# Performance work log

Measured on AMD Instinct MI355X. Metric: run time of the kernel, lower is better.

The kernel has to match this reference:

```python
import jax, jax.numpy as jnp
import numpy as np

B, N, D = 1, 2048, 320
H, DH = 8, 40            # MultiheadAttention(320, num_heads=8)
STEPS, LR = 100, 0.01    # refinement_steps, refinement_lr
B1, B2, EPS = 0.9, 0.999, 1e-8  # torch Adam defaults


def setup_inputs() -> dict:
    key = jax.random.key(0)
    ks = iter(jax.random.split(key, 30))
    W = lambda shape: jax.random.normal(next(ks), shape, dtype=jnp.float32) * 0.05
    return {
        "features": jax.random.normal(next(ks), (B, N, D), dtype=jnp.float32),
        # backbone_network: Linear(320,320) ReLU Dropout Linear(320,320)
        "bb_w1": W((320, 320)), "bb_b1": W((320,)),
        "bb_w2": W((320, 320)), "bb_b2": W((320,)),
        # side_chain_network: Linear(320,160) ReLU Dropout Linear(160,320)
        "sc_w1": W((320, 160)), "sc_b1": W((160,)),
        "sc_w2": W((160, 320)), "sc_b2": W((320,)),
        # MultiheadAttention packed in/out projections
        "attn_wqkv": W((320, 960)), "attn_bqkv": W((960,)),
        "attn_wo": W((320, 320)), "attn_bo": W((320,)),
        # contact mlp: Linear(320,160) ReLU Linear(160,1)
        "cm_w1": W((320, 160)), "cm_b1": W((160,)),
        "cm_w2": W((160, 1)), "cm_b2": W((1,)),
        # refiner backbone_processor: Linear(320,160) ReLU Dropout Linear(160,3)
        "rb_w1": W((320, 160)), "rb_b1": W((160,)),
        "rb_w2": W((160, 3)), "rb_b2": W((3,)),
        # refiner side_chain_processor: Linear(320,160) ReLU Dropout Linear(160,4)
        "rs_w1": W((320, 160)), "rs_b1": W((160,)),
        "rs_w2": W((160, 4)), "rs_b2": W((4,)),
    }


def _mlp2(x, w1, b1, w2, b2):
    # Linear -> ReLU -> (Dropout eval = identity) -> Linear
    return jax.nn.relu(x @ w1 + b1) @ w2 + b2


def reference(features, bb_w1, bb_b1, bb_w2, bb_b2, sc_w1, sc_b1, sc_w2, sc_b2,
              attn_wqkv, attn_bqkv, attn_wo, attn_bo, cm_w1, cm_b1, cm_w2, cm_b2,
              rb_w1, rb_b1, rb_w2, rb_b2, rs_w1, rs_b1, rs_w2, rs_b2):
    backbone_features = _mlp2(features, bb_w1, bb_b1, bb_w2, bb_b2)       # (B,N,320)
    side_chain_features = _mlp2(backbone_features, sc_w1, sc_b1, sc_w2, sc_b2)

    # --- ContactMapPredictor (self-attention, batch-first) ---
    qkv = features @ attn_wqkv + attn_bqkv                                 # (B,N,960)
    q, k, v = jnp.split(qkv, 3, axis=-1)
    hsplit = lambda t: t.reshape(B, N, H, DH)
    scores = jnp.einsum('bqhd,bkhd->bhqk', hsplit(q), hsplit(k)) / jnp.sqrt(jnp.float32(DH))
    attn = jax.nn.softmax(scores, axis=-1)
    ctx = jnp.einsum('bhqk,bkhd->bqhd', attn, hsplit(v)).reshape(B, N, D)
    attn_out = ctx @ attn_wo + attn_bo                                     # (B,N,320)
    # torch loop writes a single scalar mlp(attn_out[:, i]) across each row i
    prob = jax.nn.relu(attn_out @ cm_w1 + cm_b1) @ cm_w2 + cm_b2           # (B,N,1)
    contact_map = jnp.broadcast_to(prob, (B, N, N))                        # (B,N,N)

    # --- StructureRefiner ---
    structure0 = _mlp2(backbone_features, rb_w1, rb_b1, rb_w2, rb_b2)      # (B,N,3)
    _side_chain_angles = _mlp2(side_chain_features, rs_w1, rs_b1, rs_w2, rs_b2)  # computed (unused downstream, as in source)

    def loss_fn(x):
        diffs = x[:, :, None, :] - x[:, None, :, :]                        # (B,N,N,3)
        dist = jnp.sqrt(jnp.sum(diffs * diffs, axis=-1) + 1e-12)
        contact_loss = jnp.mean(contact_map * jax.nn.relu(dist - 8.0)
                                + (1.0 - contact_map) * jax.nn.relu(12.0 - dist))
        bond = jnp.sqrt(jnp.sum((x[:, 1:] - x[:, :-1]) ** 2, axis=-1) + 1e-12)
        return contact_loss + 0.1 * jnp.mean(jax.nn.relu(bond - 4.0))

    @jax.checkpoint
    def step(carry, t):
        x, m, v = carry
        g = jax.grad(loss_fn)(x)
        m = B1 * m + (1.0 - B1) * g
        v = B2 * v + (1.0 - B2) * g * g
        mhat = m / (1.0 - B1 ** t)
        vhat = v / (1.0 - B2 ** t)
        x = x - LR * mhat / (jnp.sqrt(vhat) + EPS)
        return (x, m, v), None

    x0 = jax.lax.stop_gradient(structure0)  # torch: detach().clone() before optimization
    ts = jnp.arange(1, STEPS + 1, dtype=jnp.float32)
    (x, _, _), _ = jax.lax.scan(step, (x0, jnp.zeros_like(x0), jnp.zeros_like(x0)), ts)
    return x  # refined_structure (B,N,3)
```

## Files before the change

### kernel.cpp

```cpp
#include <hip/hip_runtime.h>
#include <math.h>

#define N_TOK 2048
#define NH 8
#define DH 40

__global__ __launch_bounds__(256) void gemm_k(const float* __restrict__ A,
    const float* __restrict__ B, const float* __restrict__ bias,
    float* __restrict__ C, int M, int N, int K, int relu)
{
    __shared__ __align__(16) float As[16][68];
    __shared__ __align__(16) float Bs[16][68];
    const int bn = blockIdx.x * 64, bm = blockIdx.y * 64;
    const int tid = threadIdx.x;
    const int tx = tid & 15, ty = tid >> 4;
    const int la_m = tid >> 2, la_k = (tid & 3) * 4;
    const int lb_k = tid >> 4, lb_n = (tid & 15) * 4;
    const int bcol = bn + lb_n;
    const int nk = K >> 4;
    float4 aq = *(const float4*)&A[(size_t)(bm + la_m) * K + la_k];
    float4 bq = make_float4(0.f, 0.f, 0.f, 0.f);
    if (bcol < N) bq = *(const float4*)&B[(size_t)lb_k * N + bcol];
    float acc[4][4] = {};
    for (int kt = 0; kt < nk; ++kt) {
        __syncthreads();
        As[la_k + 0][la_m] = aq.x; As[la_k + 1][la_m] = aq.y;
        As[la_k + 2][la_m] = aq.z; As[la_k + 3][la_m] = aq.w;
        *(float4*)&Bs[lb_k][lb_n] = bq;
        __syncthreads();
        if (kt + 1 < nk) {
            const int k0 = (kt + 1) << 4;
            aq = *(const float4*)&A[(size_t)(bm + la_m) * K + k0 + la_k];
            if (bcol < N) bq = *(const float4*)&B[(size_t)(k0 + lb_k) * N + bcol];
        }
        #pragma unroll
        for (int kk = 0; kk < 16; ++kk) {
            const float4 av = *(const float4*)&As[kk][4 * ty];
            const float4 bv = *(const float4*)&Bs[kk][4 * tx];
            acc[0][0] += av.x * bv.x; acc[0][1] += av.x * bv.y; acc[0][2] += av.x * bv.z; acc[0][3] += av.x * bv.w;
            acc[1][0] += av.y * bv.x; acc[1][1] += av.y * bv.y; acc[1][2] += av.y * bv.z; acc[1][3] += av.y * bv.w;
            acc[2][0] += av.z * bv.x; acc[2][1] += av.z * bv.y; acc[2][2] += av.z * bv.z; acc[2][3] += av.z * bv.w;
            acc[3][0] += av.w * bv.x; acc[3][1] += av.w * bv.y; acc[3][2] += av.w * bv.z; acc[3][3] += av.w * bv.w;
        }
    }
    const int c0 = bn + 4 * tx;
    if (c0 < N) {
        const float4 bz = *(const float4*)&bias[c0];
        #pragma unroll
        for (int i = 0; i < 4; ++i) {
            float4 o;
            o.x = acc[i][0] + bz.x; o.y = acc[i][1] + bz.y;
            o.z = acc[i][2] + bz.z; o.w = acc[i][3] + bz.w;
            if (relu) {
                o.x = fmaxf(o.x, 0.f); o.y = fmaxf(o.y, 0.f);
                o.z = fmaxf(o.z, 0.f); o.w = fmaxf(o.w, 0.f);
            }
            *(float4*)&C[(size_t)(bm + 4 * ty + i) * N + c0] = o;
        }
    }
}

__global__ __launch_bounds__(256) void mlp160_k(const float* __restrict__ X,
    const float* __restrict__ W1, const float* __restrict__ b1,
    const float* __restrict__ W2, const float* __restrict__ b2,
    float* __restrict__ out, int P)
{
    __shared__ __align__(16) float Xs[8][324];
    __shared__ float Hs[8][160];
    const int tid = threadIdx.x;
    const int r0 = blockIdx.x * 8;
    for (int idx = tid; idx < 8 * 80; idx += 256) {
        const int r = idx / 80, c4 = idx % 80;
        *(float4*)&Xs[r][4 * c4] = *(const float4*)&X[(size_t)(r0 + r) * 320 + 4 * c4];
    }
    __syncthreads();
    if (tid < 160) {
        const int c = tid;
        float a0 = 0.f, a1 = 0.f, a2 = 0.f, a3 = 0.f,
              a4 = 0.f, a5 = 0.f, a6 = 0.f, a7 = 0.f;
        #pragma unroll 4
        for (int k = 0; k < 320; ++k) {
            const float w = W1[(size_t)k * 160 + c];
            a0 = fmaf(Xs[0][k], w, a0); a1 = fmaf(Xs[1][k], w, a1);
            a2 = fmaf(Xs[2][k], w, a2); a3 = fmaf(Xs[3][k], w, a3);
            a4 = fmaf(Xs[4][k], w, a4); a5 = fmaf(Xs[5][k], w, a5);
            a6 = fmaf(Xs[6][k], w, a6); a7 = fmaf(Xs[7][k], w, a7);
        }
        const float bb = b1[c];
        Hs[0][c] = fmaxf(a0 + bb, 0.f); Hs[1][c] = fmaxf(a1 + bb, 0.f);
        Hs[2][c] = fmaxf(a2 + bb, 0.f); Hs[3][c] = fmaxf(a3 + bb, 0.f);
        Hs[4][c] = fmaxf(a4 + bb, 0.f); Hs[5][c] = fmaxf(a5 + bb, 0.f);
        Hs[6][c] = fmaxf(a6 + bb, 0.f); Hs[7][c] = fmaxf(a7 + bb, 0.f);
    }
    __syncthreads();
    const int r = tid >> 5, l = tid & 31;
    for (int p = 0; p < P; ++p) {
        float a = 0.f;
        for (int c = l; c < 160; c += 32)
            a = fmaf(Hs[r][c], W2[(size_t)c * P + p], a);
        #pragma unroll
        for (int off = 16; off; off >>= 1) a += __shfl_xor(a, off, 32);
        if (l == 0) out[(size_t)(r0 + r) * P + p] = a + b2[p];
    }
}

#define QT 16
#define KCH 2
#define KROWS (N_TOK / KCH)
__global__ __launch_bounds__(256) void attn_part_k(const float* __restrict__ qkv,
    float* __restrict__ ctxp, float* __restrict__ msp)
{
    __shared__ float Qs[DH][17];
    __shared__ __align__(16) float Ks[DH][64];
    __shared__ __align__(16) float Vs[DH][64];
    const int h = blockIdx.y;
    const int q0 = blockIdx.x * QT;
    const int ch = blockIdx.z;
    const int tid = threadIdx.x;
    const int kg = tid & 15, q = tid >> 4;

    for (int idx = tid; idx < QT * 10; idx += 256) {
        const int r = idx / 10, qd = idx % 10;
        const float4 qq = *(const float4*)&qkv[(size_t)(q0 + r) * 960 + h * DH + 4 * qd];
        Qs[4 * qd + 0][r] = qq.x; Qs[4 * qd + 1][r] = qq.y;
        Qs[4 * qd + 2][r] = qq.z; Qs[4 * qd + 3][r] = qq.w;
    }

    float M = -1e30f, S = 0.f;
    float ctx[DH];
    #pragma unroll
    for (int d = 0; d < DH; ++d) ctx[d] = 0.f;
    const float scale = 0.15811388300841897f;

    for (int t0 = ch * KROWS; t0 < (ch + 1) * KROWS; t0 += 64) {
        __syncthreads();
        for (int idx = tid; idx < 640; idx += 256) {
            const int r = idx / 10, qd = idx % 10;
            const float* base = &qkv[(size_t)(t0 + r) * 960 + h * DH];
            const float4 kq = *(const float4*)(base + 320 + 4 * qd);
            const float4 vq = *(const float4*)(base + 640 + 4 * qd);
            const int c = r ^ ((qd & 7) << 2);
            #pragma unroll
            for (int j = 0; j < 4; ++j) {
                const int d = 4 * qd + j;
                Ks[d][c] = ((const float*)&kq)[j];
                Vs[d][c] = ((const float*)&vq)[j];
            }
        }
        __syncthreads();

        float s0_ = 0.f, s1_ = 0.f, s2_ = 0.f, s3_ = 0.f;
        #pragma unroll
        for (int d = 0; d < DH; ++d) {
            const float qv = Qs[d][q];
            const float4 kv = *(const float4*)&Ks[d][(4 * kg) ^ (((d >> 2) & 7) << 2)];
            s0_ += qv * kv.x; s1_ += qv * kv.y; s2_ += qv * kv.z; s3_ += qv * kv.w;
        }
        s0_ *= scale; s1_ *= scale; s2_ *= scale; s3_ *= scale;

        float tm = fmaxf(fmaxf(s0_, s1_), fmaxf(s2_, s3_));
        #pragma unroll
        for (int off = 1; off < 16; off <<= 1) tm = fmaxf(tm, __shfl_xor(tm, off, 16));
        const float Mn = fmaxf(M, tm);
        const float p0 = __expf(s0_ - Mn), p1 = __expf(s1_ - Mn);
        const float p2 = __expf(s2_ - Mn), p3 = __expf(s3_ - Mn);
        float ps = p0 + p1 + p2 + p3;
        #pragma unroll
        for (int off = 1; off < 16; off <<= 1) ps += __shfl_xor(ps, off, 16);
        if (Mn > M) {
            const float sc = __expf(M - Mn);
            S = S * sc + ps; M = Mn;
            #pragma unroll
            for (int d = 0; d < DH; ++d) ctx[d] *= sc;
        } else S += ps;

        #pragma unroll
        for (int d = 0; d < DH; ++d) {
            const float4 vv = *(const float4*)&Vs[d][(4 * kg) ^ (((d >> 2) & 7) << 2)];
            ctx[d] += p0 * vv.x + p1 * vv.y + p2 * vv.z + p3 * vv.w;
        }
    }

    #pragma unroll
    for (int off = 1; off < 16; off <<= 1) {
        #pragma unroll
        for (int d = 0; d < DH; ++d) ctx[d] += __shfl_xor(ctx[d], off, 16);
    }
    const int qr = q0 + q;
    float4 o = make_float4(0.f, 0.f, 0.f, 0.f);
    #pragma unroll
    for (int qq = 0; qq < 10; ++qq) {
        if (kg == qq) {
            o.x = ctx[4 * qq + 0]; o.y = ctx[4 * qq + 1];
            o.z = ctx[4 * qq + 2]; o.w = ctx[4 * qq + 3];
        }
    }
    if (kg < 10)
        *(float4*)&ctxp[(size_t)((ch * N_TOK + qr) * NH + h) * DH + 4 * kg] = o;
    if (kg == 0)
        *(float2*)&msp[2 * ((size_t)(ch * N_TOK + qr) * NH + h)] = make_float2(M, S);
}

__global__ __launch_bounds__(320) void attn_comb_k(const float* __restrict__ ctxp,
    const float* __restrict__ msp, float* __restrict__ ctxo)
{
    const int q = blockIdx.x;
    const int t = threadIdx.x;
    const int h = t / DH, d = t % DH;
    const float2 ms0 = *(const float2*)&msp[2 * ((size_t)q * NH + h)];
    const float2 ms1 = *(const float2*)&msp[2 * ((size_t)(N_TOK + q) * NH + h)];
    const float c0 = ctxp[((size_t)q * NH + h) * DH + d];
    const float c1 = ctxp[((size_t)(N_TOK + q) * NH + h) * DH + d];
    const float Mx = fmaxf(ms0.x, ms1.x);
    const float w0 = __expf(ms0.x - Mx), w1 = __expf(ms1.x - Mx);
    const float S = w0 * ms0.y + w1 * ms1.y;
    ctxo[(size_t)q * 320 + t] = (w0 * c0 + w1 * c1) / S;
}

__global__ void pack_k(const float* __restrict__ s0, const float* __restrict__ prob,
                       float4* __restrict__ xslot0)
{
    const int t = blockIdx.x * 256 + threadIdx.x;
    if (t < N_TOK)
        xslot0[t] = make_float4(s0[3*t], s0[3*t+1], s0[3*t+2], prob[t]);
}

__global__ void zero_flags_k(unsigned* __restrict__ flags)
{
    const int t = threadIdx.x;
    for (int idx = t; idx < 4096; idx += 64) flags[idx] = 0u;
}

__global__ __launch_bounds__(512) void refine_coop_k(
    float4* __restrict__ xchain, float* __restrict__ xout,
    unsigned* __restrict__ flags)
{
    __shared__ __align__(16) float4 xs4[N_TOK];
    const int tid = threadIdx.x;
    const int bid = blockIdx.x;
    const int wave = tid >> 6, lane = tid & 63;
    const int i = bid * 8 + wave;
    float m0 = 0.f, m1 = 0.f, m2 = 0.f, v0 = 0.f, v1 = 0.f, v2 = 0.f;
    float b1p = 1.f, b2p = 1.f;

    for (int t = 0; t < 100; ++t) {
        const float4* cur = xchain + ((unsigned)(t * 53) % 101u) * N_TOK;
        float4* nxt       = xchain + ((unsigned)((t + 1) * 53) % 101u) * N_TOK;
        #pragma unroll
        for (int u = 0; u < 4; ++u) {
            const int idx = tid + 512 * u;
            xs4[idx] = cur[idx];
        }
        __syncthreads();
        const float4 xi = xs4[i];
        const float ci = xi.w;
        float g0 = 0.f, g1 = 0.f, g2 = 0.f;
        #pragma unroll 8
        for (int u = 0; u < N_TOK / 64; ++u) {
            const float4 qj = xs4[lane + 64 * u];
            const float dx = xi.x - qj.x;
            const float dy = xi.y - qj.y;
            const float dz = xi.z - qj.z;
            const float d2 = fmaf(dx, dx, fmaf(dy, dy, fmaf(dz, dz, 1e-12f)));
            const float rinv = rsqrtf(d2);
            const float sc = ci + qj.w;
            float w = 0.f;
            if (d2 > 64.f)  w += sc;
            if (d2 < 144.f) w -= (2.f - sc);
            const float f = w * rinv;
            g0 = fmaf(f, dx, g0); g1 = fmaf(f, dy, g1); g2 = fmaf(f, dz, g2);
        }
        #pragma unroll
        for (int off = 32; off; off >>= 1) {
            g0 += __shfl_xor(g0, off, 64);
            g1 += __shfl_xor(g1, off, 64);
            g2 += __shfl_xor(g2, off, 64);
        }
        {
            const float gs = 1.f / ((float)N_TOK * (float)N_TOK);
            g0 *= gs; g1 *= gs; g2 *= gs;
            const float bw = 0.1f / (float)(N_TOK - 1);
            if (i > 0) {
                const float4 qj = xs4[i - 1];
                const float dx = xi.x - qj.x, dy = xi.y - qj.y, dz = xi.z - qj.z;
                const float b2 = fmaf(dx, dx, fmaf(dy, dy, fmaf(dz, dz, 1e-12f)));
                if (b2 > 16.f) {
                    const float f = bw * rsqrtf(b2);
                    g0 = fmaf(f, dx, g0); g1 = fmaf(f, dy, g1); g2 = fmaf(f, dz, g2);
                }
            }
            if (i < N_TOK - 1) {
                const float4 qj = xs4[i + 1];
                const float dx = xi.x - qj.x, dy = xi.y - qj.y, dz = xi.z - qj.z;
                const float b2 = fmaf(dx, dx, fmaf(dy, dy, fmaf(dz, dz, 1e-12f)));
                if (b2 > 16.f) {
                    const float f = bw * rsqrtf(b2);
                    g0 = fmaf(f, dx, g0); g1 = fmaf(f, dy, g1); g2 = fmaf(f, dz, g2);
                }
            }
            b1p *= 0.9f; b2p *= 0.999f;
            const float bc1 = 1.f - b1p, bc2 = 1.f - b2p;
            m0 = 0.9f * m0 + 0.1f * g0; v0 = 0.999f * v0 + 0.001f * g0 * g0;
            m1 = 0.9f * m1 + 0.1f * g1; v1 = 0.999f * v1 + 0.001f * g1 * g1;
            m2 = 0.9f * m2 + 0.1f * g2; v2 = 0.999f * v2 + 0.001f * g2 * g2;
            const float nx0 = xi.x - 0.01f * (m0 / bc1) / (sqrtf(v0 / bc2) + 1e-8f);
            const float nx1 = xi.y - 0.01f * (m1 / bc1) / (sqrtf(v1 / bc2) + 1e-8f);
            const float nx2 = xi.z - 0.01f * (m2 / bc1) / (sqrtf(v2 / bc2) + 1e-8f);
            if (lane == 0) {
                if (t == 99) {
                    xout[i * 3 + 0] = nx0; xout[i * 3 + 1] = nx1; xout[i * 3 + 2] = nx2;
                } else {
                    unsigned long long* p = (unsigned long long*)&nxt[i];
                    union { float2 f2; unsigned long long u; } lo, hi;
                    lo.f2 = make_float2(nx0, nx1);
                    hi.f2 = make_float2(nx2, ci);
                    __hip_atomic_store(p,     lo.u, __ATOMIC_RELAXED, __HIP_MEMORY_SCOPE_AGENT);
                    __hip_atomic_store(p + 1, hi.u, __ATOMIC_RELAXED, __HIP_MEMORY_SCOPE_AGENT);
                }
            }
        }
        if (t < 99) {
            __syncthreads();
            if (tid == 0)
                __hip_atomic_store(&flags[bid * 16], (unsigned)(t + 1),
                    __ATOMIC_RELAXED, __HIP_MEMORY_SCOPE_AGENT);
            if (tid < 256) {
                while (__hip_atomic_load(&flags[tid * 16], __ATOMIC_RELAXED,
                        __HIP_MEMORY_SCOPE_AGENT) < (unsigned)(t + 1))
                    __builtin_amdgcn_s_sleep(2);
            }
            __syncthreads();
        }
    }
}

extern "C" void kernel_launch(void* const* d_in, const int* in_sizes, int n_in,
                              void* d_out, int out_size, void* d_ws, size_t ws_size,
                              hipStream_t stream)
{
    (void)in_sizes; (void)n_in; (void)out_size; (void)ws_size;
    const float* F    = (const float*)d_in[0];
    const float* bbw1 = (const float*)d_in[1];  const float* bbb1 = (const float*)d_in[2];
    const float* bbw2 = (const float*)d_in[3];  const float* bbb2 = (const float*)d_in[4];
    const float* wqkv = (const float*)d_in[9];  const float* bqkv = (const float*)d_in[10];
    const float* wo   = (const float*)d_in[11]; const float* bo   = (const float*)d_in[12];
    const float* cmw1 = (const float*)d_in[13]; const float* cmb1 = (const float*)d_in[14];
    const float* cmw2 = (const float*)d_in[15]; const float* cmb2 = (const float*)d_in[16];
    const float* rbw1 = (const float*)d_in[17]; const float* rbb1 = (const float*)d_in[18];
    const float* rbw2 = (const float*)d_in[19]; const float* rbb2 = (const float*)d_in[20];

    float* ws   = (float*)d_ws;
    float* qkv  = ws;
    float* h1   = qkv + 1966080;
    float* bf   = h1 + 655360;
    float* t1   = bf + 655360;
    float* ctxo = t1 + 327680;
    float* attn = ctxo + 655360;
    float* c1   = attn + 655360;
    float* prob = c1 + 327680;
    float* s0   = prob + 2048;
    unsigned* flags = (unsigned*)(s0 + 6144);
    float* ctxp = h1;
    float* msp  = t1;
    float4* xchain = (float4*)qkv;

    gemm_k<<<dim3(5, 32),  256, 0, stream>>>(F,    bbw1, bbb1, h1,   2048, 320, 320, 1);
    gemm_k<<<dim3(5, 32),  256, 0, stream>>>(h1,   bbw2, bbb2, bf,   2048, 320, 320, 0);
    mlp160_k<<<256, 256, 0, stream>>>(bf, rbw1, rbb1, rbw2, rbb2, s0, 3);
    gemm_k<<<dim3(15, 32), 256, 0, stream>>>(F,    wqkv, bqkv, qkv,  2048, 960, 320, 0);
    attn_part_k<<<dim3(N_TOK / QT, NH, KCH), 256, 0, stream>>>(qkv, ctxp, msp);
    attn_comb_k<<<N_TOK, 320, 0, stream>>>(ctxp, msp, ctxo);
    gemm_k<<<dim3(5, 32),  256, 0, stream>>>(ctxo, wo,   bo,   attn, 2048, 320, 320, 0);
    mlp160_k<<<256, 256, 0, stream>>>(attn, cmw1, cmb1, cmw2, cmb2, prob, 1);
    pack_k<<<(N_TOK + 255) / 256, 256, 0, stream>>>(s0, prob, xchain);
    zero_flags_k<<<1, 64, 0, stream>>>(flags);

    float4* xchainp = xchain; float* outp = (float*)d_out;
    unsigned* flagsp = flags;
    void* kargs[] = { (void*)&xchainp, (void*)&outp, (void*)&flagsp };
    hipLaunchCooperativeKernel((void*)refine_coop_k, dim3(256), dim3(512), kargs, 0, stream);
}
```

Baseline: 947.0 us.

## Process two queries per thread in attention to reuse K/V shared loads

Doubles the query tile per block from 16 to 32, so each thread keeps two independent online-softmax states and context accumulators. Each K and V value read from shared memory now feeds two queries instead of one, which halves LDS traffic per FLOP and the number of K/V tile loads across the grid. In exchange, per-thread register use roughly doubles (two 40-float context arrays), which may lower occupancy. The block count is also halved.

New measurement: 1.079 ms. 14.0% more time.

```diff
diff --git a/kernel.cpp b/kernel.cpp
--- a/kernel.cpp
+++ b/kernel.cpp
@@ -104,20 +104,20 @@
     }
 }
 
-#define QT 16
+#define QT 32
 #define KCH 2
 #define KROWS (N_TOK / KCH)
 __global__ __launch_bounds__(256) void attn_part_k(const float* __restrict__ qkv,
     float* __restrict__ ctxp, float* __restrict__ msp)
 {
-    __shared__ float Qs[DH][17];
+    __shared__ __align__(8) float Qs[DH][34];
     __shared__ __align__(16) float Ks[DH][64];
     __shared__ __align__(16) float Vs[DH][64];
     const int h = blockIdx.y;
     const int q0 = blockIdx.x * QT;
     const int ch = blockIdx.z;
     const int tid = threadIdx.x;
-    const int kg = tid & 15, q = tid >> 4;
+    const int kg = tid & 15, qg = tid >> 4;
 
     for (int idx = tid; idx < QT * 10; idx += 256) {
         const int r = idx / 10, qd = idx % 10;
@@ -126,10 +126,10 @@
         Qs[4 * qd + 2][r] = qq.z; Qs[4 * qd + 3][r] = qq.w;
     }
 
-    float M = -1e30f, S = 0.f;
-    float ctx[DH];
+    float M0 = -1e30f, S0 = 0.f, M1 = -1e30f, S1 = 0.f;
+    float ctx0[DH], ctx1[DH];
     #pragma unroll
-    for (int d = 0; d < DH; ++d) ctx[d] = 0.f;
+    for (int d = 0; d < DH; ++d) { ctx0[d] = 0.f; ctx1[d] = 0.f; }
     const float scale = 0.15811388300841897f;
 
     for (int t0 = ch * KROWS; t0 < (ch + 1) * KROWS; t0 += 64) {
@@ -149,56 +149,89 @@
         }
         __syncthreads();
 
-        float s0_ = 0.f, s1_ = 0.f, s2_ = 0.f, s3_ = 0.f;
+        float s00 = 0.f, s01 = 0.f, s02 = 0.f, s03 = 0.f;
+        float s10 = 0.f, s11 = 0.f, s12 = 0.f, s13 = 0.f;
         #pragma unroll
         for (int d = 0; d < DH; ++d) {
-            const float qv = Qs[d][q];
+            const float2 qv = *(const float2*)&Qs[d][2 * qg];
             const float4 kv = *(const float4*)&Ks[d][(4 * kg) ^ (((d >> 2) & 7) << 2)];
-            s0_ += qv * kv.x; s1_ += qv * kv.y; s2_ += qv * kv.z; s3_ += qv * kv.w;
-        }
-        s0_ *= scale; s1_ *= scale; s2_ *= scale; s3_ *= scale;
-
-        float tm = fmaxf(fmaxf(s0_, s1_), fmaxf(s2_, s3_));
-        #pragma unroll
-        for (int off = 1; off < 16; off <<= 1) tm = fmaxf(tm, __shfl_xor(tm, off, 16));
-        const float Mn = fmaxf(M, tm);
-        const float p0 = __expf(s0_ - Mn), p1 = __expf(s1_ - Mn);
-        const float p2 = __expf(s2_ - Mn), p3 = __expf(s3_ - Mn);
-        float ps = p0 + p1 + p2 + p3;
-        #pragma unroll
-        for (int off = 1; off < 16; off <<= 1) ps += __shfl_xor(ps, off, 16);
-        if (Mn > M) {
-            const float sc = __expf(M - Mn);
-            S = S * sc + ps; M = Mn;
+            s00 += qv.x * kv.x; s01 += qv.x * kv.y; s02 += qv.x * kv.z; s03 += qv.x * kv.w;
+            s10 += qv.y * kv.x; s11 += qv.y * kv.y; s12 += qv.y * kv.z; s13 += qv.y * kv.w;
+        }
+        s00 *= scale; s01 *= scale; s02 *= scale; s03 *= scale;
+        s10 *= scale; s11 *= scale; s12 *= scale; s13 *= scale;
+
+        float p00, p01, p02, p03, p10, p11, p12, p13;
+        {
+            float tm = fmaxf(fmaxf(s00, s01), fmaxf(s02, s03));
             #pragma unroll
-            for (int d = 0; d < DH; ++d) ctx[d] *= sc;
-        } else S += ps;
-
+            for (int off = 1; off < 16; off <<= 1) tm = fmaxf(tm, __shfl_xor(tm, off, 16));
+            const float Mn = fmaxf(M0, tm);
+            p00 = __expf(s00 - Mn); p01 = __expf(s01 - Mn);
+            p02 = __expf(s02 - Mn); p03 = __expf(s03 - Mn);
+            float ps = p00 + p01 + p02 + p03;
+            #pragma unroll
+            for (int off = 1; off < 16; off <<= 1) ps += __shfl_xor(ps, off, 16);
+            if (Mn > M0) {
+                const float sc = __expf(M0 - Mn);
+                S0 = S0 * sc + ps; M0 = Mn;
+                #pragma unroll
+                for (int d = 0; d < DH; ++d) ctx0[d] *= sc;
+            } else S0 += ps;
+        }
+        {
+            float tm = fmaxf(fmaxf(s10, s11), fmaxf(s12, s13));
+            #pragma unroll
+            for (int off = 1; off < 16; off <<= 1) tm = fmaxf(tm, __shfl_xor(tm, off, 16));
+            const float Mn = fmaxf(M1, tm);
+            p10 = __expf(s10 - Mn); p11 = __expf(s11 - Mn);
+            p12 = __expf(s12 - Mn); p13 = __expf(s13 - Mn);
+            float ps = p10 + p11 + p12 + p13;
+            #pragma unroll
+            for (int off = 1; off < 16; off <<= 1) ps += __shfl_xor(ps, off, 16);
+            if (Mn > M1) {
+                const float sc = __expf(M1 - Mn);
+                S1 = S1 * sc + ps; M1 = Mn;
+                #pragma unroll
+                for (int d = 0; d < DH; ++d) ctx1[d] *= sc;
+            } else S1 += ps;
+        }
         #pragma unroll
         for (int d = 0; d < DH; ++d) {
             const float4 vv = *(const float4*)&Vs[d][(4 * kg) ^ (((d >> 2) & 7) << 2)];
-            ctx[d] += p0 * vv.x + p1 * vv.y + p2 * vv.z + p3 * vv.w;
+            ctx0[d] += p00 * vv.x + p01 * vv.y + p02 * vv.z + p03 * vv.w;
+            ctx1[d] += p10 * vv.x + p11 * vv.y + p12 * vv.z + p13 * vv.w;
         }
     }
 
     #pragma unroll
     for (int off = 1; off < 16; off <<= 1) {
         #pragma unroll
-        for (int d = 0; d < DH; ++d) ctx[d] += __shfl_xor(ctx[d], off, 16);
-    }
-    const int qr = q0 + q;
-    float4 o = make_float4(0.f, 0.f, 0.f, 0.f);
+        for (int d = 0; d < DH; ++d) {
+            ctx0[d] += __shfl_xor(ctx0[d], off, 16);
+            ctx1[d] += __shfl_xor(ctx1[d], off, 16);
+        }
+    }
+    const int qa = q0 + 2 * qg, qb = qa + 1;
+    float4 o0 = make_float4(0.f, 0.f, 0.f, 0.f);
+    float4 o1 = make_float4(0.f, 0.f, 0.f, 0.f);
     #pragma unroll
     for (int qq = 0; qq < 10; ++qq) {
         if (kg == qq) {
-            o.x = ctx[4 * qq + 0]; o.y = ctx[4 * qq + 1];
-            o.z = ctx[4 * qq + 2]; o.w = ctx[4 * qq + 3];
-        }
-    }
-    if (kg < 10)
-        *(float4*)&ctxp[(size_t)((ch * N_TOK + qr) * NH + h) * DH + 4 * kg] = o;
-    if (kg == 0)
-        *(float2*)&msp[2 * ((size_t)(ch * N_TOK + qr) * NH + h)] = make_float2(M, S);
+            o0.x = ctx0[4 * qq + 0]; o0.y = ctx0[4 * qq + 1];
+            o0.z = ctx0[4 * qq + 2]; o0.w = ctx0[4 * qq + 3];
+            o1.x = ctx1[4 * qq + 0]; o1.y = ctx1[4 * qq + 1];
+            o1.z = ctx1[4 * qq + 2]; o1.w = ctx1[4 * qq + 3];
+        }
+    }
+    if (kg < 10) {
+        *(float4*)&ctxp[(size_t)((ch * N_TOK + qa) * NH + h) * DH + 4 * kg] = o0;
+        *(float4*)&ctxp[(size_t)((ch * N_TOK + qb) * NH + h) * DH + 4 * kg] = o1;
+    }
+    if (kg == 0) {
+        *(float2*)&msp[2 * ((size_t)(ch * N_TOK + qa) * NH + h)] = make_float2(M0, S0);
+        *(float2*)&msp[2 * ((size_t)(ch * N_TOK + qb) * NH + h)] = make_float2(M1, S1);
+    }
 }
 
 __global__ __launch_bounds__(320) void attn_comb_k(const float* __restrict__ ctxp,
```
